# Kernel optimization log

Hardware: AMD Instinct MI355X
Metric: run time of the kernel (lower is better)

## Reference

```python
import jax, jax.numpy as jnp
import numpy as np

# Semantic hierarchy configuration (stand-in for semantic_softmax_processor)
GROUP_SIZES = [8192, 4096, 2048, 1024, 512, 256, 128, 64, 32, 16]
NORM_FACTORS = [0.1] * len(GROUP_SIZES)
TOPK_CAP = 500
TEMPERATURE = 1.0
TOTAL_CLASSES = sum(GROUP_SIZES)  # 16368
BATCH = 1024


def setup_inputs() -> dict:
    key = jax.random.key(0)
    k1, k2, k3 = jax.random.split(key, 3)
    logits = jax.random.normal(k1, (BATCH, TOTAL_CLASSES), dtype=jnp.float32)
    logits_teacher = jax.random.normal(k2, (BATCH, TOTAL_CLASSES), dtype=jnp.float32)
    targets = jax.random.randint(k3, (BATCH,), 0, TOTAL_CLASSES, dtype=jnp.int64)
    return {"logits": logits, "logits_teacher": logits_teacher, "targets": targets}


def _group_kd_loss(s_logits, t_logits, temperature):
    # s_logits, t_logits: [B, C_i] for one semantic group
    B, C = t_logits.shape
    k = min(C, TOPK_CAP)
    # teacher top-k classes (sorted, largest)
    t_top, t_idx = jax.lax.top_k(t_logits, k)                 # [B, k]
    s_top = jnp.take_along_axis(s_logits, t_idx, axis=1)      # [B, k]
    log_p = jax.nn.log_softmax(s_top / temperature, axis=1)   # student log-probs
    log_q = jax.nn.log_softmax(t_top / temperature, axis=1)   # teacher log-probs
    q = jnp.exp(log_q)
    # KL(q || p), reduction='batchmean'
    kl = jnp.sum(q * (log_q - log_p)) / B
    return kl * temperature * temperature


def reference(logits, logits_teacher, targets):
    # targets are converted to semantic targets in the original module but are
    # never used in the loss computation (dead code) -> no effect on output.
    del targets
    total = jnp.float32(0.0)
    offset = 0
    for gsize, norm in zip(GROUP_SIZES, NORM_FACTORS):
        s_i = jax.lax.slice_in_dim(logits, offset, offset + gsize, axis=1)
        t_i = jax.lax.slice_in_dim(logits_teacher, offset, offset + gsize, axis=1)
        total = total + _group_kd_loss(s_i, t_i, TEMPERATURE) * norm
        offset += gsize
    return total
```

## Files before the change

kernel.cpp:

```cpp
#include <hip/hip_runtime.h>
#include <stdint.h>
#include <float.h>

#define TOTAL 16368
#define KSEL 500
#define CAPV 1280
#define NSLOT 20
#define NBUCKET 64

__device__ __forceinline__ uint32_t fkey(float f) {
    uint32_t u = __float_as_uint(f);
    return (u & 0x80000000u) ? ~u : (u | 0x80000000u);
}
__device__ __forceinline__ float keyf(uint32_t k) {
    uint32_t u = (k & 0x80000000u) ? (k & 0x7FFFFFFFu) : ~k;
    return __uint_as_float(u);
}
__device__ __forceinline__ int lanerank(uint64_t m) {
    return __builtin_amdgcn_mbcnt_hi((uint32_t)(m >> 32),
           __builtin_amdgcn_mbcnt_lo((uint32_t)m, 0));
}
__device__ __forceinline__ int wave_sumi(int v) {
    #pragma unroll
    for (int o = 32; o > 0; o >>= 1) v += __shfl_xor(v, o, 64);
    return v;
}
__device__ __forceinline__ float wave_sumf(float v) {
    #pragma unroll
    for (int o = 32; o > 0; o >>= 1) v += __shfl_xor(v, o, 64);
    return v;
}
__device__ __forceinline__ float wave_maxf(float v) {
    #pragma unroll
    for (int o = 32; o > 0; o >>= 1) v = fmaxf(v, __shfl_xor(v, o, 64));
    return v;
}
__device__ __forceinline__ void lse_merge(float& m, float& l, float m2, float l2) {
    float M = fmaxf(m, m2);
    l = l * __expf(m - M) + l2 * __expf(m2 - M);
    m = M;
}

__device__ __noinline__ float wave_slow_kl(const float* __restrict__ t,
                                           const float* __restrict__ s, int C) {
    const int lane = threadIdx.x & 63;
    uint64_t lo = 0ull, hi = (1ull << 45), tau = 0ull;
    int cl = C, ch = 0;
    #pragma unroll 1
    for (int it = 0; it < 100; ++it) {
        uint64_t span = hi - lo;
        if (span <= 1ull) { tau = lo; break; }
        uint64_t mid;
        if (it & 1) mid = lo + (span >> 1);
        else {
            uint64_t st = span * (uint64_t)(cl - KSEL) / (uint64_t)(cl - ch);
            if (st < 1) st = 1;
            if (st > span - 1) st = span - 1;
            mid = lo + st;
        }
        int c = 0;
        #pragma unroll 1
        for (int i = lane; i < C; i += 64) {
            uint64_t ck = ((uint64_t)fkey(t[i]) << 13) | (uint64_t)(8191 - i);
            c += (ck > mid);
        }
        c = wave_sumi(c);
        if (c == KSEL) { tau = mid; break; }
        if (c > KSEL) { lo = mid; cl = c; } else { hi = mid; ch = c; }
    }
    float tmx = -FLT_MAX;
    for (int i = lane; i < C; i += 64) tmx = fmaxf(tmx, t[i]);
    tmx = wave_maxf(tmx);
    float St = 0.f, Stt = 0.f, Sts = 0.f, sm = -FLT_MAX;
    #pragma unroll 1
    for (int i = lane; i < C; i += 64) {
        float x = t[i];
        uint64_t ck = ((uint64_t)fkey(x) << 13) | (uint64_t)(8191 - i);
        if (ck > tau) {
            float e = __expf(x - tmx), v = s[i];
            St += e; Stt += e * x; Sts += e * v;
            sm = fmaxf(sm, v);
        }
    }
    St = wave_sumf(St); Stt = wave_sumf(Stt); Sts = wave_sumf(Sts); sm = wave_maxf(sm);
    float Ss = 0.f;
    #pragma unroll 1
    for (int i = lane; i < C; i += 64) {
        uint64_t ck = ((uint64_t)fkey(t[i]) << 13) | (uint64_t)(8191 - i);
        if (ck > tau) Ss += __expf(s[i] - sm);
    }
    Ss = wave_sumf(Ss);
    if (lane == 0)
        return (Stt - Sts) / St - tmx - __logf(St) + sm + __logf(Ss);
    return 0.f;
}

template <int NF4>
__device__ float big_wave(const float* __restrict__ tg, const float* __restrict__ sg,
                          float thr, uint32_t* kv, float* sv) {
    const int lane = threadIdx.x & 63;
    const float4* t4 = (const float4*)tg;
    const float4* s4 = (const float4*)sg;
    constexpr int NB = NF4 / 4;
    constexpr int C = NF4 * 256;
    int cnt = 0;
    float4 tb[4], sb[4], tn[4], sn[4];
    #pragma unroll
    for (int u = 0; u < 4; ++u) { tb[u] = t4[u * 64 + lane]; sb[u] = s4[u * 64 + lane]; }
    #pragma unroll 1
    for (int b = 0; b < NB; ++b) {
        if (b + 1 < NB) {
            #pragma unroll
            for (int u = 0; u < 4; ++u) {
                tn[u] = t4[((b + 1) * 4 + u) * 64 + lane];
                sn[u] = s4[((b + 1) * 4 + u) * 64 + lane];
            }
        }
        #pragma unroll
        for (int u = 0; u < 4; ++u) {
            float tx[4] = {tb[u].x, tb[u].y, tb[u].z, tb[u].w};
            float sx[4] = {sb[u].x, sb[u].y, sb[u].z, sb[u].w};
            #pragma unroll
            for (int q = 0; q < 4; ++q) {
                bool p = tx[q] > thr;
                uint64_t m = __ballot(p);
                if (p) {
                    int ofs = cnt + lanerank(m);
                    if (ofs < CAPV) { kv[ofs] = fkey(tx[q]); sv[ofs] = sx[q]; }
                }
                cnt += (int)__popcll(m);
            }
        }
        if (b + 1 < NB) {
            #pragma unroll
            for (int u = 0; u < 4; ++u) { tb[u] = tn[u]; sb[u] = sn[u]; }
        }
    }
    if (cnt < KSEL || cnt > CAPV) return wave_slow_kl(tg, sg, C);

    for (int p = cnt + lane; p < CAPV; p += 64) kv[p] = 0u;
    uint32_t key[NSLOT];
    float svc[NSLOT];
    #pragma unroll
    for (int j = 0; j < NSLOT; ++j) {
        int p = lane + j * 64;
        key[j] = kv[p];
        svc[j] = (p < cnt) ? sv[p] : 0.f;
    }
    uint32_t kmx = 0u, kmn = 0xFFFFFFFFu;
    #pragma unroll
    for (int j = 0; j < NSLOT; ++j) {
        uint32_t k = key[j];
        kmx = k > kmx ? k : kmx;
        if (k) kmn = k < kmn ? k : kmn;
    }
    #pragma unroll
    for (int o = 32; o > 0; o >>= 1) {
        uint32_t a = __shfl_xor(kmx, o, 64); kmx = a > kmx ? a : kmx;
        uint32_t b2 = __shfl_xor(kmn, o, 64); kmn = b2 < kmn ? b2 : kmn;
    }
    const float tmax = keyf(kmx);

    uint32_t lo = kmn - 1u, hi = kmx, tauhi = kmx;
    int cl = cnt, ch = 0;
    bool exact = false, tiesAll = false;
    int tieN = 0;
    #pragma unroll 1
    for (int it = 0; it < 80; ++it) {
        uint32_t span = hi - lo;
        if (span <= 1u) break;
        uint32_t mid;
        if (!(it & 1)) {
            uint64_t st = (uint64_t)span * (uint32_t)(cl - KSEL) / (uint32_t)(cl - ch);
            if (st < 1) st = 1;
            if (st > span - 1) st = span - 1;
            mid = lo + (uint32_t)st;
        } else mid = lo + (span >> 1);
        int c = 0;
        #pragma unroll
        for (int j = 0; j < NSLOT; ++j)
            c += (int)__popcll(__ballot(key[j] > mid));
        if (c == KSEL) { tauhi = mid; exact = true; break; }
        if (c > KSEL) { lo = mid; cl = c; } else { hi = mid; ch = c; }
    }
    if (!exact) {
        tauhi = hi;
        const int nT = KSEL - ch, nTie = cl - ch;
        if (nT >= nTie) tiesAll = true;
        else tieN = nT;
    }

    float St = 0.f, Stt = 0.f, Sts = 0.f, sm = -FLT_MAX;
    #pragma unroll
    for (int j = 0; j < NSLOT; ++j) {
        bool sj = tiesAll ? (key[j] >= tauhi) : (key[j] > tauhi);
        if (sj) {
            float tv = keyf(key[j]);
            float e = __expf(tv - tmax);
            St += e; Stt += e * tv; Sts += e * svc[j];
            sm = fmaxf(sm, svc[j]);
        }
    }
    if (tieN > 0) {
        int rem = tieN;
        #pragma unroll 1
        for (int base = 0; base < C && rem > 0; base += 64) {
            float tvv = tg[base + lane];
            bool tie = (fkey(tvv) == tauhi);
            uint64_t m = __ballot(tie);
            if (tie && lanerank(m) < rem) {
                float e = __expf(tvv - tmax);
                float svv = sg[base + lane];
                St += e; Stt += e * tvv; Sts += e * svv;
                sm = fmaxf(sm, svv);
            }
            int pc = (int)__popcll(m);
            rem = (pc >= rem) ? 0 : (rem - pc);
        }
    }
    #pragma unroll
    for (int o = 32; o > 0; o >>= 1) {
        St  += __shfl_xor(St,  o, 64);
        Stt += __shfl_xor(Stt, o, 64);
        Sts += __shfl_xor(Sts, o, 64);
        sm = fmaxf(sm, __shfl_xor(sm, o, 64));
    }
    float Ss = 0.f;
    #pragma unroll
    for (int j = 0; j < NSLOT; ++j) {
        bool sj = tiesAll ? (key[j] >= tauhi) : (key[j] > tauhi);
        if (sj) Ss += __expf(svc[j] - sm);
    }
    if (tieN > 0) {
        int rem = tieN;
        #pragma unroll 1
        for (int base = 0; base < C && rem > 0; base += 64) {
            float tvv = tg[base + lane];
            bool tie = (fkey(tvv) == tauhi);
            uint64_t m = __ballot(tie);
            if (tie && lanerank(m) < rem)
                Ss += __expf(sg[base + lane] - sm);
            int pc = (int)__popcll(m);
            rem = (pc >= rem) ? 0 : (rem - pc);
        }
    }
    Ss = wave_sumf(Ss);
    if (lane == 0)
        return (Stt - Sts) / St - tmax - __logf(St) + sm + __logf(Ss);
    return 0.f;
}

template <int NS, class IdxF>
__device__ float select_accum(uint32_t (&key)[NS], IdxF idxOf, const float* svp) {
    const int lane = threadIdx.x & 63;
    uint32_t kmx = 0u, kmn = 0xFFFFFFFFu;
    #pragma unroll
    for (int j = 0; j < NS; ++j) {
        uint32_t k = key[j];
        kmx = k > kmx ? k : kmx;
        kmn = k < kmn ? k : kmn;
    }
    #pragma unroll
    for (int o = 32; o > 0; o >>= 1) {
        uint32_t a = __shfl_xor(kmx, o, 64); kmx = a > kmx ? a : kmx;
        uint32_t b = __shfl_xor(kmn, o, 64); kmn = b < kmn ? b : kmn;
    }
    const float tmax = keyf(kmx);

    uint32_t lo = kmn - 1u, hi = kmx, tauhi = kmx;
    int cl = NS * 64, ch = 0, cut = -1;
    bool exact = false;
    #pragma unroll 1
    for (int it = 0; it < 80; ++it) {
        uint32_t span = hi - lo;
        if (span <= 1u) break;
        uint32_t mid;
        if (!(it & 1)) {
            uint64_t st = (uint64_t)span * (uint32_t)(cl - KSEL) / (uint32_t)(cl - ch);
            if (st < 1) st = 1;
            if (st > span - 1) st = span - 1;
            mid = lo + (uint32_t)st;
        } else mid = lo + (span >> 1);
        int c = 0;
        #pragma unroll
        for (int j = 0; j < NS; ++j)
            c += (int)__popcll(__ballot(key[j] > mid));
        if (c == KSEL) { tauhi = mid; exact = true; break; }
        if (c > KSEL) { lo = mid; cl = c; } else { hi = mid; ch = c; }
    }
    if (!exact) {
        tauhi = hi;
        const int nT = KSEL - ch, nTie = cl - ch;
        if (nT >= nTie) cut = 0x7FFFFFFF;
        else {
            int l = -1, h = NS * 64 - 1;
            #pragma unroll 1
            while (h - l > 1) {
                int m = (l + h) >> 1;
                int c = 0;
                #pragma unroll
                for (int j = 0; j < NS; ++j)
                    c += (int)__popcll(__ballot(key[j] == tauhi && idxOf(j) <= m));
                if (c >= nT) h = m; else l = m;
            }
            cut = h;
        }
    }

    float St = 0.f, Stt = 0.f, Sts = 0.f, sm = -FLT_MAX;
    #pragma unroll
    for (int j = 0; j < NS; ++j) {
        uint32_t kj = key[j];
        bool sj = (kj > tauhi) || (kj == tauhi && idxOf(j) <= cut);
        if (sj) {
            float tv = keyf(kj);
            float e = __expf(tv - tmax);
            St += e; Stt += e * tv; Sts += e * svp[j];
            sm = fmaxf(sm, svp[j]);
        }
    }
    #pragma unroll
    for (int o = 32; o > 0; o >>= 1) {
        St  += __shfl_xor(St,  o, 64);
        Stt += __shfl_xor(Stt, o, 64);
        Sts += __shfl_xor(Sts, o, 64);
        sm = fmaxf(sm, __shfl_xor(sm, o, 64));
    }
    float Ss = 0.f;
    #pragma unroll
    for (int j = 0; j < NS; ++j) {
        uint32_t kj = key[j];
        bool sj = (kj > tauhi) || (kj == tauhi && idxOf(j) <= cut);
        if (sj) Ss += __expf(svp[j] - sm);
    }
    Ss = wave_sumf(Ss);
    if (lane == 0)
        return (Stt - Sts) / St - tmax - __logf(St) + sm + __logf(Ss);
    return 0.f;
}

template <int NJ>
__device__ float mid_wave(const float* __restrict__ t, const float* __restrict__ s) {
    const int lane = threadIdx.x & 63;
    const float4* t4 = (const float4*)t;
    const float4* s4 = (const float4*)s;
    uint32_t key[NJ];
    float svp[NJ];
    #pragma unroll
    for (int c = 0; c < NJ / 4; ++c) {
        float4 x = t4[lane + c * 64];
        float4 y = s4[lane + c * 64];
        key[4 * c + 0] = fkey(x.x); key[4 * c + 1] = fkey(x.y);
        key[4 * c + 2] = fkey(x.z); key[4 * c + 3] = fkey(x.w);
        svp[4 * c + 0] = y.x; svp[4 * c + 1] = y.y;
        svp[4 * c + 2] = y.z; svp[4 * c + 3] = y.w;
    }
    auto idxOf = [&](int j) { return ((lane + (j >> 2) * 64) << 2) + (j & 3); };
    return select_accum<NJ>(key, idxOf, svp);
}

__device__ float tiny_group(const float* __restrict__ t, const float* __restrict__ s,
                            int Cg) {
    const int lane = threadIdx.x & 63;
    float St = 0.f, Stt = 0.f, Sts = 0.f, m = -FLT_MAX, l = 0.f;
    float tv[4], svv[4];
    #pragma unroll
    for (int q = 0; q < 4; ++q) {
        int i = lane + q * 64;
        bool va = i < Cg;
        tv[q] = va ? t[i] : -FLT_MAX;
        svv[q] = va ? s[i] : 0.f;
    }
    float mx = -FLT_MAX;
    #pragma unroll
    for (int q = 0; q < 4; ++q) mx = fmaxf(mx, tv[q]);
    mx = wave_maxf(mx);
    #pragma unroll
    for (int q = 0; q < 4; ++q) {
        if (lane + q * 64 < Cg) {
            float e = __expf(tv[q] - mx);
            St += e; Stt += e * tv[q]; Sts += e * svv[q];
            float x = svv[q];
            if (x > m) { l = l * __expf(m - x) + 1.f; m = x; }
            else       { l += __expf(x - m); }
        }
    }
    #pragma unroll
    for (int o = 32; o > 0; o >>= 1) {
        St  += __shfl_xor(St,  o, 64);
        Stt += __shfl_xor(Stt, o, 64);
        Sts += __shfl_xor(Sts, o, 64);
        float m2 = __shfl_xor(m, o, 64);
        float l2 = __shfl_xor(l, o, 64);
        lse_merge(m, l, m2, l2);
    }
    if (lane == 0)
        return (Stt - Sts) / St - mx - __logf(St) + m + __logf(l);
    return 0.f;
}

__global__ __launch_bounds__(64, 4) void kd_jobs(const float* __restrict__ sL,
                                                 const float* __restrict__ tL,
                                                 float* __restrict__ partial) {
    __shared__ uint32_t kv[CAPV];
    __shared__ float    sv[CAPV];
    const int bid = blockIdx.x;
    const int job = bid >> 10;
    const int row = bid & 1023;
    const float* tr = tL + (size_t)row * TOTAL;
    const float* sr = sL + (size_t)row * TOTAL;

    float kl = 0.f;
    switch (job) {
    case 0:
        kl = big_wave<32>(tr, sr, 1.10f, kv, sv);
        break;
    case 1:
        kl = big_wave<16>(tr + 8192, sr + 8192, 0.60f, kv, sv);
        break;
    case 2:
        kl = big_wave<8>(tr + 12288, sr + 12288, 0.50f, kv, sv);
        break;
    case 3:
        kl = mid_wave<16>(tr + 14336, sr + 14336);
        break;
    default:
        kl  = mid_wave<8>(tr + 15360, sr + 15360);
        kl += tiny_group(tr + 15872, sr + 15872, 256);
        kl += tiny_group(tr + 16128, sr + 16128, 128);
        kl += tiny_group(tr + 16256, sr + 16256, 64);
        kl += tiny_group(tr + 16320, sr + 16320, 32);
        kl += tiny_group(tr + 16352, sr + 16352, 16);
        break;
    }

    if ((threadIdx.x & 63) == 0)
        atomicAdd(&partial[(row + job * 37) & (NBUCKET - 1)], kl * (0.1f / 1024.f));
}

__global__ void zero_ws(float* partial) {
    if (threadIdx.x < NBUCKET) partial[threadIdx.x] = 0.f;
}

__global__ void final_sum(const float* __restrict__ partial, float* __restrict__ out) {
    float v = (threadIdx.x < NBUCKET) ? partial[threadIdx.x] : 0.f;
    #pragma unroll
    for (int o = 32; o > 0; o >>= 1) v += __shfl_down(v, o, 64);
    if (threadIdx.x == 0) out[0] = v;
}

extern "C" void kernel_launch(void* const* d_in, const int* in_sizes, int n_in,
                              void* d_out, int out_size, void* d_ws, size_t ws_size,
                              hipStream_t stream) {
    (void)in_sizes; (void)n_in; (void)ws_size; (void)out_size;
    const float* s = (const float*)d_in[0];
    const float* t = (const float*)d_in[1];
    float* out = (float*)d_out;
    float* ws = (float*)d_ws;

    hipLaunchKernelGGL(zero_ws, dim3(1), dim3(64), 0, stream, ws);
    hipLaunchKernelGGL(kd_jobs, dim3(5120), dim3(64), 0, stream, s, t, ws);
    hipLaunchKernelGGL(final_sum, dim3(1), dim3(64), 0, stream, ws, out);
}
```

Baseline: 171.8 us.

## Split large-group top-k into parallel slice compaction and a separate select kernel

The two largest groups (8192 and 4096 columns) are no longer handled by one wave per row streaming the whole group. They are now compacted by several waves per row, each thresholding a 2048-column slice into global workspace, and a second kernel merges the per-slice candidates and runs the key-threshold selection. This aims to cut the long per-row critical path that limited the old single-kernel schedule, and to raise occupancy with launch bounds of 8. The cost is an extra launch and a global round trip for the candidates, and the path depends on workspace size, falling back to the old kernel if it is too small. mid_wave also drops its index-ordered tie handling in favour of the shared keysel routine.

Result: slower. 223.0 us (+29.8%).

```diff
diff --git a/kernel.cpp b/kernel.cpp
--- a/kernel.cpp
+++ b/kernel.cpp
@@ -4,9 +4,18 @@
 
 #define TOTAL 16368
 #define KSEL 500
-#define CAPV 1280
-#define NSLOT 20
 #define NBUCKET 64
+
+#define CNT_OFF_F 64
+#define P0_OFF 33024
+#define Q0CAP 384
+#define Q0NS 24
+#define Q1CAP 704
+#define Q1NS 22
+#define G2CAP 768
+#define G2NS 12
+#define CAPJ 1280
+#define NSJ 20
 
 __device__ __forceinline__ uint32_t fkey(float f) {
     uint32_t u = __float_as_uint(f);
@@ -95,61 +104,14 @@
     return 0.f;
 }
 
-template <int NF4>
-__device__ float big_wave(const float* __restrict__ tg, const float* __restrict__ sg,
-                          float thr, uint32_t* kv, float* sv) {
-    const int lane = threadIdx.x & 63;
-    const float4* t4 = (const float4*)tg;
-    const float4* s4 = (const float4*)sg;
-    constexpr int NB = NF4 / 4;
-    constexpr int C = NF4 * 256;
-    int cnt = 0;
-    float4 tb[4], sb[4], tn[4], sn[4];
-    #pragma unroll
-    for (int u = 0; u < 4; ++u) { tb[u] = t4[u * 64 + lane]; sb[u] = s4[u * 64 + lane]; }
-    #pragma unroll 1
-    for (int b = 0; b < NB; ++b) {
-        if (b + 1 < NB) {
-            #pragma unroll
-            for (int u = 0; u < 4; ++u) {
-                tn[u] = t4[((b + 1) * 4 + u) * 64 + lane];
-                sn[u] = s4[((b + 1) * 4 + u) * 64 + lane];
-            }
-        }
-        #pragma unroll
-        for (int u = 0; u < 4; ++u) {
-            float tx[4] = {tb[u].x, tb[u].y, tb[u].z, tb[u].w};
-            float sx[4] = {sb[u].x, sb[u].y, sb[u].z, sb[u].w};
-            #pragma unroll
-            for (int q = 0; q < 4; ++q) {
-                bool p = tx[q] > thr;
-                uint64_t m = __ballot(p);
-                if (p) {
-                    int ofs = cnt + lanerank(m);
-                    if (ofs < CAPV) { kv[ofs] = fkey(tx[q]); sv[ofs] = sx[q]; }
-                }
-                cnt += (int)__popcll(m);
-            }
-        }
-        if (b + 1 < NB) {
-            #pragma unroll
-            for (int u = 0; u < 4; ++u) { tb[u] = tn[u]; sb[u] = sn[u]; }
-        }
-    }
-    if (cnt < KSEL || cnt > CAPV) return wave_slow_kl(tg, sg, C);
-
-    for (int p = cnt + lane; p < CAPV; p += 64) kv[p] = 0u;
-    uint32_t key[NSLOT];
-    float svc[NSLOT];
-    #pragma unroll
-    for (int j = 0; j < NSLOT; ++j) {
-        int p = lane + j * 64;
-        key[j] = kv[p];
-        svc[j] = (p < cnt) ? sv[p] : 0.f;
-    }
+template <int NS>
+__device__ float keysel_kl(uint32_t (&key)[NS], float (&svc)[NS], int tot,
+                           const float* __restrict__ tg,
+                           const float* __restrict__ sg, int C) {
+    const int lane = threadIdx.x & 63;
     uint32_t kmx = 0u, kmn = 0xFFFFFFFFu;
     #pragma unroll
-    for (int j = 0; j < NSLOT; ++j) {
+    for (int j = 0; j < NS; ++j) {
         uint32_t k = key[j];
         kmx = k > kmx ? k : kmx;
         if (k) kmn = k < kmn ? k : kmn;
@@ -162,114 +124,9 @@
     const float tmax = keyf(kmx);
 
     uint32_t lo = kmn - 1u, hi = kmx, tauhi = kmx;
-    int cl = cnt, ch = 0;
+    int cl = tot, ch = 0;
     bool exact = false, tiesAll = false;
     int tieN = 0;
-    #pragma unroll 1
-    for (int it = 0; it < 80; ++it) {
-        uint32_t span = hi - lo;
-        if (span <= 1u) break;
-        uint32_t mid;
-        if (!(it & 1)) {
-            uint64_t st = (uint64_t)span * (uint32_t)(cl - KSEL) / (uint32_t)(cl - ch);
-            if (st < 1) st = 1;
-            if (st > span - 1) st = span - 1;
-            mid = lo + (uint32_t)st;
-        } else mid = lo + (span >> 1);
-        int c = 0;
-        #pragma unroll
-        for (int j = 0; j < NSLOT; ++j)
-            c += (int)__popcll(__ballot(key[j] > mid));
-        if (c == KSEL) { tauhi = mid; exact = true; break; }
-        if (c > KSEL) { lo = mid; cl = c; } else { hi = mid; ch = c; }
-    }
-    if (!exact) {
-        tauhi = hi;
-        const int nT = KSEL - ch, nTie = cl - ch;
-        if (nT >= nTie) tiesAll = true;
-        else tieN = nT;
-    }
-
-    float St = 0.f, Stt = 0.f, Sts = 0.f, sm = -FLT_MAX;
-    #pragma unroll
-    for (int j = 0; j < NSLOT; ++j) {
-        bool sj = tiesAll ? (key[j] >= tauhi) : (key[j] > tauhi);
-        if (sj) {
-            float tv = keyf(key[j]);
-            float e = __expf(tv - tmax);
-            St += e; Stt += e * tv; Sts += e * svc[j];
-            sm = fmaxf(sm, svc[j]);
-        }
-    }
-    if (tieN > 0) {
-        int rem = tieN;
-        #pragma unroll 1
-        for (int base = 0; base < C && rem > 0; base += 64) {
-            float tvv = tg[base + lane];
-            bool tie = (fkey(tvv) == tauhi);
-            uint64_t m = __ballot(tie);
-            if (tie && lanerank(m) < rem) {
-                float e = __expf(tvv - tmax);
-                float svv = sg[base + lane];
-                St += e; Stt += e * tvv; Sts += e * svv;
-                sm = fmaxf(sm, svv);
-            }
-            int pc = (int)__popcll(m);
-            rem = (pc >= rem) ? 0 : (rem - pc);
-        }
-    }
-    #pragma unroll
-    for (int o = 32; o > 0; o >>= 1) {
-        St  += __shfl_xor(St,  o, 64);
-        Stt += __shfl_xor(Stt, o, 64);
-        Sts += __shfl_xor(Sts, o, 64);
-        sm = fmaxf(sm, __shfl_xor(sm, o, 64));
-    }
-    float Ss = 0.f;
-    #pragma unroll
-    for (int j = 0; j < NSLOT; ++j) {
-        bool sj = tiesAll ? (key[j] >= tauhi) : (key[j] > tauhi);
-        if (sj) Ss += __expf(svc[j] - sm);
-    }
-    if (tieN > 0) {
-        int rem = tieN;
-        #pragma unroll 1
-        for (int base = 0; base < C && rem > 0; base += 64) {
-            float tvv = tg[base + lane];
-            bool tie = (fkey(tvv) == tauhi);
-            uint64_t m = __ballot(tie);
-            if (tie && lanerank(m) < rem)
-                Ss += __expf(sg[base + lane] - sm);
-            int pc = (int)__popcll(m);
-            rem = (pc >= rem) ? 0 : (rem - pc);
-        }
-    }
-    Ss = wave_sumf(Ss);
-    if (lane == 0)
-        return (Stt - Sts) / St - tmax - __logf(St) + sm + __logf(Ss);
-    return 0.f;
-}
-
-template <int NS, class IdxF>
-__device__ float select_accum(uint32_t (&key)[NS], IdxF idxOf, const float* svp) {
-    const int lane = threadIdx.x & 63;
-    uint32_t kmx = 0u, kmn = 0xFFFFFFFFu;
-    #pragma unroll
-    for (int j = 0; j < NS; ++j) {
-        uint32_t k = key[j];
-        kmx = k > kmx ? k : kmx;
-        kmn = k < kmn ? k : kmn;
-    }
-    #pragma unroll
-    for (int o = 32; o > 0; o >>= 1) {
-        uint32_t a = __shfl_xor(kmx, o, 64); kmx = a > kmx ? a : kmx;
-        uint32_t b = __shfl_xor(kmn, o, 64); kmn = b < kmn ? b : kmn;
-    }
-    const float tmax = keyf(kmx);
-
-    uint32_t lo = kmn - 1u, hi = kmx, tauhi = kmx;
-    int cl = NS * 64, ch = 0, cut = -1;
-    bool exact = false;
     #pragma unroll 1
     for (int it = 0; it < 80; ++it) {
         uint32_t span = hi - lo;
@@ -291,32 +148,36 @@
     if (!exact) {
         tauhi = hi;
         const int nT = KSEL - ch, nTie = cl - ch;
-        if (nT >= nTie) cut = 0x7FFFFFFF;
-        else {
-            int l = -1, h = NS * 64 - 1;
-            #pragma unroll 1
-            while (h - l > 1) {
-                int m = (l + h) >> 1;
-                int c = 0;
-                #pragma unroll
-                for (int j = 0; j < NS; ++j)
-                    c += (int)__popcll(__ballot(key[j] == tauhi && idxOf(j) <= m));
-                if (c >= nT) h = m; else l = m;
+        if (nT >= nTie) tiesAll = true;
+        else tieN = nT;
+    }
+
+    float St = 0.f, Stt = 0.f, Sts = 0.f, sm = -FLT_MAX;
+    #pragma unroll
+    for (int j = 0; j < NS; ++j) {
+        bool sj = tiesAll ? (key[j] >= tauhi) : (key[j] > tauhi);
+        if (sj) {
+            float tv = keyf(key[j]);
+            float e = __expf(tv - tmax);
+            St += e; Stt += e * tv; Sts += e * svc[j];
+            sm = fmaxf(sm, svc[j]);
+        }
+    }
+    if (tieN > 0) {
+        int rem = tieN;
+        #pragma unroll 1
+        for (int base = 0; base < C && rem > 0; base += 64) {
+            float tvv = tg[base + lane];
+            bool tie = (fkey(tvv) == tauhi);
+            uint64_t m = __ballot(tie);
+            if (tie && lanerank(m) < rem) {
+                float e = __expf(tvv - tmax);
+                float svv = sg[base + lane];
+                St += e; Stt += e * tvv; Sts += e * svv;
+                sm = fmaxf(sm, svv);
             }
-            cut = h;
-        }
-    }
-
-    float St = 0.f, Stt = 0.f, Sts = 0.f, sm = -FLT_MAX;
-    #pragma unroll
-    for (int j = 0; j < NS; ++j) {
-        uint32_t kj = key[j];
-        bool sj = (kj > tauhi) || (kj == tauhi && idxOf(j) <= cut);
-        if (sj) {
-            float tv = keyf(kj);
-            float e = __expf(tv - tmax);
-            St += e; Stt += e * tv; Sts += e * svp[j];
-            sm = fmaxf(sm, svp[j]);
+            int pc = (int)__popcll(m);
+            rem = (pc >= rem) ? 0 : (rem - pc);
         }
     }
     #pragma unroll
@@ -329,14 +190,144 @@
     float Ss = 0.f;
     #pragma unroll
     for (int j = 0; j < NS; ++j) {
-        uint32_t kj = key[j];
-        bool sj = (kj > tauhi) || (kj == tauhi && idxOf(j) <= cut);
-        if (sj) Ss += __expf(svp[j] - sm);
+        bool sj = tiesAll ? (key[j] >= tauhi) : (key[j] > tauhi);
+        if (sj) Ss += __expf(svc[j] - sm);
+    }
+    if (tieN > 0) {
+        int rem = tieN;
+        #pragma unroll 1
+        for (int base = 0; base < C && rem > 0; base += 64) {
+            float tvv = tg[base + lane];
+            bool tie = (fkey(tvv) == tauhi);
+            uint64_t m = __ballot(tie);
+            if (tie && lanerank(m) < rem)
+                Ss += __expf(sg[base + lane] - sm);
+            int pc = (int)__popcll(m);
+            rem = (pc >= rem) ? 0 : (rem - pc);
+        }
     }
     Ss = wave_sumf(Ss);
     if (lane == 0)
         return (Stt - Sts) / St - tmax - __logf(St) + sm + __logf(Ss);
     return 0.f;
+}
+
+template <int NF4, int CAPT, int NS>
+__device__ float big_wave(const float* __restrict__ tg, const float* __restrict__ sg,
+                          float thr, uint32_t* kv, float* sv) {
+    const int lane = threadIdx.x & 63;
+    const float4* t4 = (const float4*)tg;
+    const float4* s4 = (const float4*)sg;
+    constexpr int NB = NF4 / 4;
+    constexpr int C = NF4 * 256;
+    int cnt = 0;
+    float4 tb[4], sb[4], tn[4], sn[4];
+    #pragma unroll
+    for (int u = 0; u < 4; ++u) { tb[u] = t4[u * 64 + lane]; sb[u] = s4[u * 64 + lane]; }
+    #pragma unroll 1
+    for (int b = 0; b < NB; ++b) {
+        if (b + 1 < NB) {
+            #pragma unroll
+            for (int u = 0; u < 4; ++u) {
+                tn[u] = t4[((b + 1) * 4 + u) * 64 + lane];
+                sn[u] = s4[((b + 1) * 4 + u) * 64 + lane];
+            }
+        }
+        #pragma unroll
+        for (int u = 0; u < 4; ++u) {
+            float tx[4] = {tb[u].x, tb[u].y, tb[u].z, tb[u].w};
+            float sx[4] = {sb[u].x, sb[u].y, sb[u].z, sb[u].w};
+            #pragma unroll
+            for (int q = 0; q < 4; ++q) {
+                bool p = tx[q] > thr;
+                uint64_t m = __ballot(p);
+                if (p) {
+                    int ofs = cnt + lanerank(m);
+                    if (ofs < CAPT) { kv[ofs] = fkey(tx[q]); sv[ofs] = sx[q]; }
+                }
+                cnt += (int)__popcll(m);
+            }
+        }
+        if (b + 1 < NB) {
+            #pragma unroll
+            for (int u = 0; u < 4; ++u) { tb[u] = tn[u]; sb[u] = sn[u]; }
+        }
+    }
+    if (cnt < KSEL || cnt > CAPT) return wave_slow_kl(tg, sg, C);
+
+    for (int p = cnt + lane; p < CAPT; p += 64) kv[p] = 0u;
+    uint32_t key[NS];
+    float svc[NS];
+    #pragma unroll
+    for (int j = 0; j < NS; ++j) {
+        int p = lane + j * 64;
+        key[j] = kv[p];
+        svc[j] = (p < cnt) ? sv[p] : 0.f;
+    }
+    return keysel_kl<NS>(key, svc, cnt, tg, sg, C);
+}
+
+__device__ void slice_compact(const float* __restrict__ tg,
+                              const float* __restrict__ sg,
+                              float thr, int cap, uint2* __restrict__ out,
+                              int* __restrict__ cnt_out) {
+    const int lane = threadIdx.x & 63;
+    const float4* t4 = (const float4*)tg;
+    const float4* s4 = (const float4*)sg;
+    float4 tb[8], sb[8];
+    #pragma unroll
+    for (int u = 0; u < 8; ++u) tb[u] = t4[u * 64 + lane];
+    #pragma unroll
+    for (int u = 0; u < 8; ++u) sb[u] = s4[u * 64 + lane];
+    int cnt = 0;
+    #pragma unroll
+    for (int u = 0; u < 8; ++u) {
+        float tx[4] = {tb[u].x, tb[u].y, tb[u].z, tb[u].w};
+        float sx[4] = {sb[u].x, sb[u].y, sb[u].z, sb[u].w};
+        #pragma unroll
+        for (int q = 0; q < 4; ++q) {
+            bool p = tx[q] > thr;
+            uint64_t m = __ballot(p);
+            if (p) {
+                int ofs = cnt + lanerank(m);
+                if (ofs < cap)
+                    out[ofs] = make_uint2(fkey(tx[q]), __float_as_uint(sx[q]));
+            }
+            cnt += (int)__popcll(m);
+        }
+    }
+    if (lane == 0) *cnt_out = cnt;
+}
+
+template <int S, int CAPQ, int NS>
+__device__ float group_select(const uint2* __restrict__ pairs,
+                              const int* __restrict__ cnts, int C,
+                              const float* __restrict__ tg,
+                              const float* __restrict__ sg) {
+    const int lane = threadIdx.x & 63;
+    int cq[S];
+    int tot = 0; bool bad = false;
+    #pragma unroll
+    for (int q = 0; q < S; ++q) {
+        cq[q] = cnts[q];
+        tot += cq[q];
+        bad = bad || (cq[q] > CAPQ);
+    }
+    if (bad || tot < KSEL) return wave_slow_kl(tg, sg, C);
+
+    constexpr int SP = CAPQ / 64;
+    uint32_t key[NS];
+    float svc[NS];
+    #pragma unroll
+    for (int j = 0; j < NS; ++j) {
+        int q = j / SP;
+        int i = (j % SP) * 64 + lane;
+        bool v = i < cq[q];
+        uint2 pr = v ? pairs[q * CAPQ + i] : make_uint2(0u, 0u);
+        key[j] = pr.x;
+        svc[j] = __uint_as_float(pr.y);
+    }
+    return keysel_kl<NS>(key, svc, tot, tg, sg, C);
 }
 
 template <int NJ>
@@ -355,8 +346,7 @@
         svp[4 * c + 0] = y.x; svp[4 * c + 1] = y.y;
         svp[4 * c + 2] = y.z; svp[4 * c + 3] = y.w;
     }
-    auto idxOf = [&](int j) { return ((lane + (j >> 2) * 64) << 2) + (j & 3); };
-    return select_accum<NJ>(key, idxOf, svp);
+    return keysel_kl<NJ>(key, svp, NJ * 64, t, s, NJ * 64);
 }
 
 __device__ float tiny_group(const float* __restrict__ t, const float* __restrict__ s,
@@ -399,11 +389,88 @@
     return 0.f;
 }
 
+__global__ __launch_bounds__(64, 8) void kd_compact(const float* __restrict__ sL,
+                                                    const float* __restrict__ tL,
+                                                    float* __restrict__ ws) {
+    __shared__ uint32_t kv2[G2CAP];
+    __shared__ float    sv2[G2CAP];
+    int* cnts = (int*)(ws + CNT_OFF_F);
+    uint2* g0p = (uint2*)((char*)ws + P0_OFF);
+    uint2* g1p = g0p + (size_t)1024 * 4 * Q0CAP;
+    const int bid = blockIdx.x;
+
+    if (bid < 1024) {
+        const int row = bid;
+        const float* tr = tL + (size_t)row * TOTAL;
+        const float* sr = sL + (size_t)row * TOTAL;
+        float kl = big_wave<8, G2CAP, G2NS>(tr + 12288, sr + 12288, 0.50f, kv2, sv2);
+        if ((threadIdx.x & 63) == 0)
+            atomicAdd(&ws[(row + 74) & (NBUCKET - 1)], kl * (0.1f / 1024.f));
+    } else if (bid < 5120) {
+        const int u = bid - 1024, row = u >> 2, q = u & 3;
+        const float* tr = tL + (size_t)row * TOTAL;
+        const float* sr = sL + (size_t)row * TOTAL;
+        slice_compact(tr + q * 2048, sr + q * 2048, 1.10f, Q0CAP,
+                      g0p + ((size_t)row * 4 + q) * Q0CAP, &cnts[row * 8 + q]);
+    } else if (bid < 7168) {
+        const int u = bid - 5120, row = u >> 1, q = u & 1;
+        const float* tr = tL + (size_t)row * TOTAL;
+        const float* sr = sL + (size_t)row * TOTAL;
+        slice_compact(tr + 8192 + q * 2048, sr + 8192 + q * 2048, 0.60f, Q1CAP,
+                      g1p + ((size_t)row * 2 + q) * Q1CAP, &cnts[row * 8 + 4 + q]);
+    } else if (bid < 8192) {
+        const int row = bid - 7168;
+        const float* tr = tL + (size_t)row * TOTAL;
+        const float* sr = sL + (size_t)row * TOTAL;
+        float kl = mid_wave<16>(tr + 14336, sr + 14336);
+        if ((threadIdx.x & 63) == 0)
+            atomicAdd(&ws[(row + 111) & (NBUCKET - 1)], kl * (0.1f / 1024.f));
+    } else {
+        const int row = bid - 8192;
+        const float* tr = tL + (size_t)row * TOTAL;
+        const float* sr = sL + (size_t)row * TOTAL;
+        float kl  = mid_wave<8>(tr + 15360, sr + 15360);
+        kl += tiny_group(tr + 15872, sr + 15872, 256);
+        kl += tiny_group(tr + 16128, sr + 16128, 128);
+        kl += tiny_group(tr + 16256, sr + 16256, 64);
+        kl += tiny_group(tr + 16320, sr + 16320, 32);
+        kl += tiny_group(tr + 16352, sr + 16352, 16);
+        if ((threadIdx.x & 63) == 0)
+            atomicAdd(&ws[(row + 148) & (NBUCKET - 1)], kl * (0.1f / 1024.f));
+    }
+}
+
+__global__ __launch_bounds__(64, 8) void kd_select(const float* __restrict__ sL,
+                                                   const float* __restrict__ tL,
+                                                   float* __restrict__ ws) {
+    int* cnts = (int*)(ws + CNT_OFF_F);
+    uint2* g0p = (uint2*)((char*)ws + P0_OFF);
+    uint2* g1p = g0p + (size_t)1024 * 4 * Q0CAP;
+    const int bid = blockIdx.x;
+    float kl;
+    int row, job;
+    if (bid < 1024) {
+        row = bid; job = 0;
+        const float* tr = tL + (size_t)row * TOTAL;
+        const float* sr = sL + (size_t)row * TOTAL;
+        kl = group_select<4, Q0CAP, Q0NS>(g0p + (size_t)row * 4 * Q0CAP,
+                                          cnts + row * 8, 8192, tr, sr);
+    } else {
+        row = bid - 1024; job = 1;
+        const float* tr = tL + (size_t)row * TOTAL + 8192;
+        const float* sr = sL + (size_t)row * TOTAL + 8192;
+        kl = group_select<2, Q1CAP, Q1NS>(g1p + (size_t)row * 2 * Q1CAP,
+                                          cnts + row * 8 + 4, 4096, tr, sr);
+    }
+    if ((threadIdx.x & 63) == 0)
+        atomicAdd(&ws[(row + job * 37) & (NBUCKET - 1)], kl * (0.1f / 1024.f));
+}
+
 __global__ __launch_bounds__(64, 4) void kd_jobs(const float* __restrict__ sL,
                                                  const float* __restrict__ tL,
                                                  float* __restrict__ partial) {
-    __shared__ uint32_t kv[CAPV];
-    __shared__ float    sv[CAPV];
+    __shared__ uint32_t kv[CAPJ];
+    __shared__ float    sv[CAPJ];
     const int bid = blockIdx.x;
     const int job = bid >> 10;
     const int row = bid & 1023;
@@ -413,13 +480,13 @@
     float kl = 0.f;
     switch (job) {
     case 0:
-        kl = big_wave<32>(tr, sr, 1.10f, kv, sv);
+        kl = big_wave<32, CAPJ, NSJ>(tr, sr, 1.10f, kv, sv);
         break;
     case 1:
-        kl = big_wave<16>(tr + 8192, sr + 8192, 0.60f, kv, sv);
+        kl = big_wave<16, CAPJ, NSJ>(tr + 8192, sr + 8192, 0.60f, kv, sv);
         break;
     case 2:
-        kl = big_wave<8>(tr + 12288, sr + 12288, 0.50f, kv, sv);
+        kl = big_wave<8, CAPJ, NSJ>(tr + 12288, sr + 12288, 0.50f, kv, sv);
         break;
     case 3:
         kl = mid_wave<16>(tr + 14336, sr + 14336);
@@ -433,7 +500,6 @@
         kl += tiny_group(tr + 16352, sr + 16352, 16);
         break;
     }
-
     if ((threadIdx.x & 63) == 0)
         atomicAdd(&partial[(row + job * 37) & (NBUCKET - 1)], kl * (0.1f / 1024.f));
 }
@@ -452,13 +518,22 @@
 extern "C" void kernel_launch(void* const* d_in, const int* in_sizes, int n_in,
                               void* d_out, int out_size, void* d_ws, size_t ws_size,
                               hipStream_t stream) {
-    (void)in_sizes; (void)n_in; (void)ws_size; (void)out_size;
+    (void)in_sizes; (void)n_in; (void)out_size;
     const float* s = (const float*)d_in[0];
     const float* t = (const float*)d_in[1];
     float* out = (float*)d_out;
     float* ws = (float*)d_ws;
 
+    const size_t need = (size_t)P0_OFF +
+                        (size_t)1024 * 4 * Q0CAP * 8 +
+                        (size_t)1024 * 2 * Q1CAP * 8;
+
     hipLaunchKernelGGL(zero_ws, dim3(1), dim3(64), 0, stream, ws);
-    hipLaunchKernelGGL(kd_jobs, dim3(5120), dim3(64), 0, stream, s, t, ws);
+    if (ws_size >= need) {
+        hipLaunchKernelGGL(kd_compact, dim3(9216), dim3(64), 0, stream, s, t, ws);
+        hipLaunchKernelGGL(kd_select, dim3(2048), dim3(64), 0, stream, s, t, ws);
+    } else {
+        hipLaunchKernelGGL(kd_jobs, dim3(5120), dim3(64), 0, stream, s, t, ws);
+    }
     hipLaunchKernelGGL(final_sum, dim3(1), dim3(64), 0, stream, ws, out);
 }
```
